# Kernel optimization log

Hardware: AMD Instinct MI355X
Metric: run time of the kernel (lower is better)

The kernel has to match this reference:

```python
import jax, jax.numpy as jnp
import numpy as np

ALPHA = 0.1   # alpha_factor
BETA = 1.0    # beta_factor
NUM_CLASSES = 1000
B, D = 4096, 512


def setup_inputs() -> dict:
    key = jax.random.key(0)
    ks = jax.random.split(key, 7)
    return {
        "anchor": jax.random.normal(ks[0], (B, D), dtype=jnp.float32),
        "positive": jax.random.normal(ks[1], (B, D), dtype=jnp.float32),
        "negative": jax.random.normal(ks[2], (B, D), dtype=jnp.float32),
        "outputs": jax.random.normal(ks[3], (3 * B, NUM_CLASSES), dtype=jnp.float32),
        "labels_anchor": jax.random.randint(ks[4], (B,), 0, NUM_CLASSES, dtype=jnp.int32).astype(jnp.int64),
        "labels_neg": jax.random.randint(ks[5], (B,), 0, NUM_CLASSES, dtype=jnp.int32).astype(jnp.int64),
        "exemplars": jax.random.normal(ks[6], (NUM_CLASSES, D), dtype=jnp.float32),
    }


def reference(anchor, positive, negative, outputs, labels_anchor, labels_neg, exemplars):
    # cross-entropy (mean reduction) over concatenated labels [3B]
    labels = jnp.concatenate([labels_anchor, labels_anchor, labels_neg], axis=0)
    logp = jax.nn.log_softmax(outputs, axis=-1)                       # [3B, C]
    loss_softmax = -jnp.mean(jnp.take_along_axis(logp, labels[:, None], axis=1))

    # pairwise L2 distances anchor-to-exemplars via ||a||^2 + ||e||^2 - 2 a.e  -> [B, C]
    a_sq = jnp.sum(anchor * anchor, axis=1, keepdims=True)            # [B, 1]
    e_sq = jnp.sum(exemplars * exemplars, axis=1)[None, :]            # [1, C]
    d2 = a_sq + e_sq - 2.0 * (anchor @ exemplars.T)                   # [B, C]
    d_all = jnp.sqrt(jnp.maximum(d2, 0.0))

    d_ref = jnp.take_along_axis(d_all, labels_anchor[:, None], axis=1)[:, 0]  # [B]
    d_closest = jnp.min(d_all, axis=1)                                # [B]
    loss_center = jnp.sum(jax.nn.relu(d_ref - d_closest))

    tp = jnp.linalg.norm(anchor - positive, axis=1)                   # [B]
    tn = jnp.linalg.norm(anchor - negative, axis=1)                   # [B]
    loss_triplet = jnp.sum(jax.nn.relu(tp - tn))

    loss_total = loss_softmax + ALPHA * loss_center + BETA * loss_triplet
    return (loss_total, loss_triplet, loss_softmax, loss_center)
```

## Files before the change

### kernel.cpp

```cpp
#include <hip/hip_runtime.h>
#include <math.h>

#define BB 4096
#define DD 512
#define CC 1000

typedef __attribute__((ext_vector_type(8))) short short8;
typedef __attribute__((ext_vector_type(4))) float f32x4;

#define OFF_ABF   0
#define OFF_EBF   1048576
#define OFF_ESQ   1310720
#define OFF_ASQ   1311744
#define OFF_DREF  1315840
#define OFF_PMINP 1319936
#define OFF_CEP   1352704
#define OFF_TRP   1354240

__device__ __forceinline__ unsigned short f2bf(float x) {
    unsigned u = __float_as_uint(x);
    unsigned r = (u + 0x7FFFu + ((u >> 16) & 1u)) >> 16;
    return (unsigned short)r;
}

__global__ __launch_bounds__(512) void prep_kernel(
    const float* __restrict__ a, const float* __restrict__ ex,
    unsigned short* __restrict__ Abf, unsigned short* __restrict__ Ebf,
    float* __restrict__ esq, float* __restrict__ asq)
{
    const int bid = blockIdx.x;
    const int tid = threadIdx.x;
    const int w = tid >> 6, lane = tid & 63;

    if (bid < 512) {
        const int i = bid * 8 + w;
        const float4* ar = (const float4*)(a + (size_t)i * DD);
        float sa = 0.f;
#pragma unroll
        for (int k = 0; k < 2; k++) {
            const int j = lane + k * 64;
            float4 av = ar[j];
            union { unsigned short u[4]; uint2 q; } o;
            o.u[0]=f2bf(av.x); o.u[1]=f2bf(av.y); o.u[2]=f2bf(av.z); o.u[3]=f2bf(av.w);
            *(uint2*)(Abf + (size_t)i * DD + j * 4) = o.q;
            sa += av.x*av.x + av.y*av.y + av.z*av.z + av.w*av.w;
        }
        for (int off = 32; off; off >>= 1) sa += __shfl_xor(sa, off);
        if (lane == 0) asq[i] = sa;
    } else {
        const int c = (bid - 512) * 8 + w;
        float s = 0.f;
        if (c < CC) {
            const float4* row = (const float4*)(ex + (size_t)c * DD);
#pragma unroll
            for (int k = 0; k < 2; k++) {
                const int j = lane + k * 64;
                float4 v = row[j];
                union { unsigned short u[4]; uint2 q; } o;
                o.u[0]=f2bf(v.x); o.u[1]=f2bf(v.y); o.u[2]=f2bf(v.z); o.u[3]=f2bf(v.w);
                *(uint2*)(Ebf + (size_t)c * DD + j * 4) = o.q;
                s += v.x*v.x + v.y*v.y + v.z*v.z + v.w*v.w;
            }
            for (int off = 32; off; off >>= 1) s += __shfl_xor(s, off);
        } else {
            const uint2 z = make_uint2(0, 0);
#pragma unroll
            for (int k = 0; k < 2; k++) {
                const int j = lane + k * 64;
                *(uint2*)(Ebf + (size_t)c * DD + j * 4) = z;
            }
        }
        if (lane == 0) esq[c] = s;
    }
}

#define GL2LDS(gsrc, ldst) __builtin_amdgcn_global_load_lds( \
    (const __attribute__((address_space(1))) unsigned int*)(gsrc), \
    (__attribute__((address_space(3))) unsigned int*)(ldst), 16, 0, 0)

__global__ __launch_bounds__(512) void main_kernel(
    const unsigned short* __restrict__ Ab, const unsigned short* __restrict__ Eb,
    const float* __restrict__ asq, const float* __restrict__ esq,
    const float* __restrict__ a, const float* __restrict__ p,
    const float* __restrict__ n, const float* __restrict__ ex,
    const float* __restrict__ outp,
    const int* __restrict__ la, const int* __restrict__ ln,
    float* __restrict__ pminp, float* __restrict__ ce_part,
    float* __restrict__ tr_part, float* __restrict__ dref)
{
    __shared__ unsigned short lA[3][128 * 32];
    __shared__ unsigned short lB[3][128 * 32];
    __shared__ float s_pm[4][128];
    __shared__ float ps[8];

    const int bid = blockIdx.x;
    const int tid = threadIdx.x;
    const int w = tid >> 6, lane = tid & 63;

    if (bid < 256) {
        const int strip = bid & 31, panel = bid >> 5;
        const int gm0 = strip * 128, gn0 = panel * 128;
        const int wm = w >> 2, wn = w & 3;
        const int hi = lane >> 4, lo = lane & 15;

        const int r0 = tid >> 2, s0 = tid & 3;
        const int g0 = s0 ^ (r0 & 3);
        const size_t srcA = ((size_t)(gm0 + r0) << 9) + (g0 << 3);
        const size_t srcB = ((size_t)(gn0 + r0) << 9) + (g0 << 3);
        const int dst = tid << 3;

#define STAGE(buf, kt) do { \
        GL2LDS(Ab + srcA + ((kt) << 5), &lA[buf][dst]); \
        GL2LDS(Eb + srcB + ((kt) << 5), &lB[buf][dst]); \
    } while (0)

        f32x4 acc[4][2];
#pragma unroll
        for (int mi = 0; mi < 4; mi++)
#pragma unroll
            for (int ni = 0; ni < 2; ni++) acc[mi][ni] = (f32x4){0.f, 0.f, 0.f, 0.f};

        STAGE(0, 0);
        STAGE(1, 1);
        for (int kt = 0; kt < 16; kt++) {
            const int buf = kt % 3;
            if (kt < 14) {
                STAGE((kt + 2) % 3, kt + 2);
                asm volatile("s_waitcnt vmcnt(4)" ::: "memory");
            } else if (kt == 14) {
                asm volatile("s_waitcnt vmcnt(2)" ::: "memory");
            } else {
                asm volatile("s_waitcnt vmcnt(0)" ::: "memory");
            }
            __builtin_amdgcn_s_barrier();
            asm volatile("" ::: "memory");

            short8 af[4], bf[2];
#pragma unroll
            for (int mi = 0; mi < 4; mi++) {
                int r = (wm << 6) + (mi << 4) + lo;
                af[mi] = *(const short8*)&lA[buf][(r << 5) + ((hi ^ (r & 3)) << 3)];
            }
#pragma unroll
            for (int ni = 0; ni < 2; ni++) {
                int r = (wn << 5) + (ni << 4) + lo;
                bf[ni] = *(const short8*)&lB[buf][(r << 5) + ((hi ^ (r & 3)) << 3)];
            }
#pragma unroll
            for (int mi = 0; mi < 4; mi++)
#pragma unroll
                for (int ni = 0; ni < 2; ni++)
                    acc[mi][ni] = __builtin_amdgcn_mfma_f32_16x16x32_bf16(af[mi], bf[ni], acc[mi][ni], 0, 0, 0);

            asm volatile("" ::: "memory");
            __builtin_amdgcn_s_barrier();
        }
#undef STAGE

        float aq[4][4];
#pragma unroll
        for (int mi = 0; mi < 4; mi++) {
            float4 a0 = *(const float4*)&asq[gm0 + wm * 64 + mi * 16 + hi * 4];
            aq[mi][0]=a0.x; aq[mi][1]=a0.y; aq[mi][2]=a0.z; aq[mi][3]=a0.w;
        }
        float esqc[2]; int bad[2];
#pragma unroll
        for (int ni = 0; ni < 2; ni++) {
            int gn = gn0 + wn * 32 + ni * 16 + lo;
            esqc[ni] = esq[gn];
            bad[ni] = (gn >= CC);
        }
        float vmin[4][4];
#pragma unroll
        for (int mi = 0; mi < 4; mi++)
#pragma unroll
            for (int j = 0; j < 4; j++) {
                float best = INFINITY;
#pragma unroll
                for (int ni = 0; ni < 2; ni++) {
                    float d2 = aq[mi][j] + esqc[ni] - 2.f * acc[mi][ni][j];
                    float d = sqrtf(fmaxf(d2, 0.f));
                    if (bad[ni]) d = INFINITY;
                    best = fminf(best, d);
                }
                vmin[mi][j] = best;
            }
#pragma unroll
        for (int off = 1; off < 16; off <<= 1)
#pragma unroll
            for (int mi = 0; mi < 4; mi++)
#pragma unroll
                for (int j = 0; j < 4; j++)
                    vmin[mi][j] = fminf(vmin[mi][j], __shfl_xor(vmin[mi][j], off));

        if (lo == 0) {
#pragma unroll
            for (int mi = 0; mi < 4; mi++)
#pragma unroll
                for (int j = 0; j < 4; j++)
                    s_pm[wn][wm * 64 + mi * 16 + hi * 4 + j] = vmin[mi][j];
        }
        __syncthreads();
        if (tid < 128) {
            float m2 = fminf(fminf(s_pm[0][tid], s_pm[1][tid]),
                             fminf(s_pm[2][tid], s_pm[3][tid]));
            pminp[((size_t)(gm0 + tid) << 3) + panel] = m2;
        }
    } else if (bid < 1792) {
        const int cb = bid - 256;
        const int r = cb * 8 + w;
        const int label = (r < 2 * BB) ? la[r & (BB - 1)] : ln[r - 2 * BB];
        const float4* row4 = (const float4*)(outp + (size_t)r * CC);
        float4 v[4];
#pragma unroll
        for (int k = 0; k < 4; k++) {
            int j4 = lane + k * 64;
            v[k] = (j4 < 250) ? row4[j4]
                              : make_float4(-INFINITY, -INFINITY, -INFINITY, -INFINITY);
        }
        float m = -INFINITY;
#pragma unroll
        for (int k = 0; k < 4; k++)
            m = fmaxf(m, fmaxf(fmaxf(v[k].x, v[k].y), fmaxf(v[k].z, v[k].w)));
        for (int off = 32; off; off >>= 1) m = fmaxf(m, __shfl_xor(m, off));

        const int lj4 = label >> 2, lc = label & 3;
        float s = 0.f, lv = 0.f;
#pragma unroll
        for (int k = 0; k < 4; k++) {
            int j4 = lane + k * 64;
            s += __expf(v[k].x - m) + __expf(v[k].y - m)
               + __expf(v[k].z - m) + __expf(v[k].w - m);
            float comp = (lc == 0) ? v[k].x : (lc == 1) ? v[k].y : (lc == 2) ? v[k].z : v[k].w;
            lv += (j4 == lj4) ? comp : 0.f;
        }
        for (int off = 32; off; off >>= 1) {
            s += __shfl_xor(s, off);
            lv += __shfl_xor(lv, off);
        }
        if (lane == 0) ps[w] = -(lv - m - __logf(s));
        __syncthreads();
        if (tid == 0) {
            float t = 0.f;
#pragma unroll
            for (int q = 0; q < 8; q++) t += ps[q];
            ce_part[cb] = t;
        }
    } else {
        const int i = (bid - 1792) * 8 + w;
        const int label = la[i];
        const float4* ar = (const float4*)(a + (size_t)i * DD);
        const float4* pr = (const float4*)(p + (size_t)i * DD);
        const float4* nr = (const float4*)(n + (size_t)i * DD);
        const float4* er = (const float4*)(ex + (size_t)label * DD);
        float sp = 0.f, sn = 0.f, se = 0.f;
#pragma unroll
        for (int k = 0; k < 2; k++) {
            const int j = lane + k * 64;
            float4 av = ar[j], pv = pr[j], nv = nr[j], ev = er[j];
            float dx = av.x-pv.x, dy = av.y-pv.y, dz = av.z-pv.z, dw = av.w-pv.w;
            sp += dx*dx + dy*dy + dz*dz + dw*dw;
            dx = av.x-nv.x; dy = av.y-nv.y; dz = av.z-nv.z; dw = av.w-nv.w;
            sn += dx*dx + dy*dy + dz*dz + dw*dw;
            dx = av.x-ev.x; dy = av.y-ev.y; dz = av.z-ev.z; dw = av.w-ev.w;
            se += dx*dx + dy*dy + dz*dz + dw*dw;
        }
        for (int off = 32; off; off >>= 1) {
            sp += __shfl_xor(sp, off);
            sn += __shfl_xor(sn, off);
            se += __shfl_xor(se, off);
        }
        if (lane == 0) {
            dref[i] = sqrtf(se);
            ps[w] = fmaxf(sqrtf(sp) - sqrtf(sn), 0.f);
        }
        __syncthreads();
        if (tid == 0) {
            float t = 0.f;
#pragma unroll
            for (int q = 0; q < 8; q++) t += ps[q];
            tr_part[bid - 1792] = t;
        }
    }
}

__global__ __launch_bounds__(1024) void final_kernel(
    const float* __restrict__ ce_part, const float* __restrict__ tr_part,
    const float* __restrict__ pminp, const float* __restrict__ dref,
    float* __restrict__ out)
{
    int tid = threadIdx.x;
    float ce = ce_part[tid] + ((tid < 512) ? ce_part[tid + 1024] : 0.f);
    float tr = (tid < 512) ? tr_part[tid] : 0.f;
    float ctr = 0.f;
    float4 d4 = *(const float4*)&dref[tid * 4];
#pragma unroll
    for (int k = 0; k < 4; k++) {
        int m = tid * 4 + k;
        float4 p0 = *(const float4*)&pminp[(size_t)m * 8];
        float4 p1 = *(const float4*)&pminp[(size_t)m * 8 + 4];
        float mn = fminf(fminf(fminf(p0.x, p0.y), fminf(p0.z, p0.w)),
                         fminf(fminf(p1.x, p1.y), fminf(p1.z, p1.w)));
        float dr = (k == 0) ? d4.x : (k == 1) ? d4.y : (k == 2) ? d4.z : d4.w;
        ctr += fmaxf(dr - mn, 0.f);
    }
    for (int off = 32; off; off >>= 1) {
        ce += __shfl_xor(ce, off);
        tr += __shfl_xor(tr, off);
        ctr += __shfl_xor(ctr, off);
    }
    __shared__ float s[3][16];
    int wid = tid >> 6, lane = tid & 63;
    if (lane == 0) { s[0][wid] = ce; s[1][wid] = tr; s[2][wid] = ctr; }
    __syncthreads();
    if (tid == 0) {
        float tce = 0.f, ttr = 0.f, tctr = 0.f;
#pragma unroll
        for (int q = 0; q < 16; q++) { tce += s[0][q]; ttr += s[1][q]; tctr += s[2][q]; }
        float lsm = tce / (3.f * BB);
        out[0] = lsm + 0.1f * tctr + 1.0f * ttr;
        out[1] = ttr;
        out[2] = lsm;
        out[3] = tctr;
    }
}

extern "C" void kernel_launch(void* const* d_in, const int* in_sizes, int n_in,
                              void* d_out, int out_size, void* d_ws, size_t ws_size,
                              hipStream_t stream) {
    const float* anchor   = (const float*)d_in[0];
    const float* positive = (const float*)d_in[1];
    const float* negative = (const float*)d_in[2];
    const float* outputs  = (const float*)d_in[3];
    const int*   la       = (const int*)d_in[4];
    const int*   ln       = (const int*)d_in[5];
    const float* ex       = (const float*)d_in[6];
    float* out = (float*)d_out;
    float* ws  = (float*)d_ws;

    unsigned short* Abf = (unsigned short*)(ws + OFF_ABF);
    unsigned short* Ebf = (unsigned short*)(ws + OFF_EBF);
    float* esq      = ws + OFF_ESQ;
    float* asq      = ws + OFF_ASQ;
    float* dref     = ws + OFF_DREF;
    float* pminp    = ws + OFF_PMINP;
    float* ce_part  = ws + OFF_CEP;
    float* tr_part  = ws + OFF_TRP;

    hipLaunchKernelGGL(prep_kernel,  dim3(640),  dim3(512),  0, stream,
                       anchor, ex, Abf, Ebf, esq, asq);
    hipLaunchKernelGGL(main_kernel,  dim3(2304), dim3(512),  0, stream,
                       Abf, Ebf, asq, esq, anchor, positive, negative, ex,
                       outputs, la, ln, pminp, ce_part, tr_part, dref);
    hipLaunchKernelGGL(final_kernel, dim3(1),    dim3(1024), 0, stream,
                       ce_part, tr_part, pminp, dref, out);
}
```

Measured before the change: 32.98 us.

## Fuse triplet/dref work into prep kernel and load GEMM fragments directly from global

The triplet and reference-distance computation moves into the prep kernel's anchor blocks, which already read the anchor rows, so the anchor is read once instead of twice and main_kernel has fewer blocks. The GEMM path drops its LDS triple-buffered global_load_lds pipeline and barriers. Each wave now loads its bf16 MFMA fragments straight from global memory, relying on L2/L1 for reuse. This removes the LDS usage and synchronisation, at the cost of redundant global loads across waves and less latency hiding.

Measured after the change: 46.08 us. 39.7% more time.

```diff
diff --git a/kernel.cpp b/kernel.cpp
--- a/kernel.cpp
+++ b/kernel.cpp
@@ -24,29 +24,59 @@
 }
 
 __global__ __launch_bounds__(512) void prep_kernel(
-    const float* __restrict__ a, const float* __restrict__ ex,
+    const float* __restrict__ a, const float* __restrict__ p,
+    const float* __restrict__ n, const float* __restrict__ ex,
+    const int* __restrict__ la,
     unsigned short* __restrict__ Abf, unsigned short* __restrict__ Ebf,
-    float* __restrict__ esq, float* __restrict__ asq)
+    float* __restrict__ esq, float* __restrict__ asq,
+    float* __restrict__ dref, float* __restrict__ tr_part)
 {
+    __shared__ float ps[8];
     const int bid = blockIdx.x;
     const int tid = threadIdx.x;
     const int w = tid >> 6, lane = tid & 63;
 
     if (bid < 512) {
         const int i = bid * 8 + w;
+        const int label = la[i];
         const float4* ar = (const float4*)(a + (size_t)i * DD);
-        float sa = 0.f;
+        const float4* pr = (const float4*)(p + (size_t)i * DD);
+        const float4* nr = (const float4*)(n + (size_t)i * DD);
+        const float4* er = (const float4*)(ex + (size_t)label * DD);
+        float sa = 0.f, sp = 0.f, sn = 0.f, se = 0.f;
 #pragma unroll
         for (int k = 0; k < 2; k++) {
             const int j = lane + k * 64;
-            float4 av = ar[j];
+            float4 av = ar[j], pv = pr[j], nv = nr[j], ev = er[j];
             union { unsigned short u[4]; uint2 q; } o;
             o.u[0]=f2bf(av.x); o.u[1]=f2bf(av.y); o.u[2]=f2bf(av.z); o.u[3]=f2bf(av.w);
             *(uint2*)(Abf + (size_t)i * DD + j * 4) = o.q;
             sa += av.x*av.x + av.y*av.y + av.z*av.z + av.w*av.w;
-        }
-        for (int off = 32; off; off >>= 1) sa += __shfl_xor(sa, off);
-        if (lane == 0) asq[i] = sa;
+            float dx = av.x-pv.x, dy = av.y-pv.y, dz = av.z-pv.z, dw = av.w-pv.w;
+            sp += dx*dx + dy*dy + dz*dz + dw*dw;
+            dx = av.x-nv.x; dy = av.y-nv.y; dz = av.z-nv.z; dw = av.w-nv.w;
+            sn += dx*dx + dy*dy + dz*dz + dw*dw;
+            dx = av.x-ev.x; dy = av.y-ev.y; dz = av.z-ev.z; dw = av.w-ev.w;
+            se += dx*dx + dy*dy + dz*dz + dw*dw;
+        }
+        for (int off = 32; off; off >>= 1) {
+            sa += __shfl_xor(sa, off);
+            sp += __shfl_xor(sp, off);
+            sn += __shfl_xor(sn, off);
+            se += __shfl_xor(se, off);
+        }
+        if (lane == 0) {
+            asq[i]  = sa;
+            dref[i] = sqrtf(se);
+            ps[w] = fmaxf(sqrtf(sp) - sqrtf(sn), 0.f);
+        }
+        __syncthreads();
+        if (tid == 0) {
+            float t = 0.f;
+#pragma unroll
+            for (int q = 0; q < 8; q++) t += ps[q];
+            tr_part[bid] = t;
+        }
     } else {
         const int c = (bid - 512) * 8 + w;
         float s = 0.f;
@@ -74,22 +104,13 @@
     }
 }
 
-#define GL2LDS(gsrc, ldst) __builtin_amdgcn_global_load_lds( \
-    (const __attribute__((address_space(1))) unsigned int*)(gsrc), \
-    (__attribute__((address_space(3))) unsigned int*)(ldst), 16, 0, 0)
-
 __global__ __launch_bounds__(512) void main_kernel(
     const unsigned short* __restrict__ Ab, const unsigned short* __restrict__ Eb,
     const float* __restrict__ asq, const float* __restrict__ esq,
-    const float* __restrict__ a, const float* __restrict__ p,
-    const float* __restrict__ n, const float* __restrict__ ex,
     const float* __restrict__ outp,
     const int* __restrict__ la, const int* __restrict__ ln,
-    float* __restrict__ pminp, float* __restrict__ ce_part,
-    float* __restrict__ tr_part, float* __restrict__ dref)
+    float* __restrict__ pminp, float* __restrict__ ce_part)
 {
-    __shared__ unsigned short lA[3][128 * 32];
-    __shared__ unsigned short lB[3][128 * 32];
     __shared__ float s_pm[4][128];
     __shared__ float ps[8];
 
@@ -103,16 +124,14 @@
         const int wm = w >> 2, wn = w & 3;
         const int hi = lane >> 4, lo = lane & 15;
 
-        const int r0 = tid >> 2, s0 = tid & 3;
-        const int g0 = s0 ^ (r0 & 3);
-        const size_t srcA = ((size_t)(gm0 + r0) << 9) + (g0 << 3);
-        const size_t srcB = ((size_t)(gn0 + r0) << 9) + (g0 << 3);
-        const int dst = tid << 3;
-
-#define STAGE(buf, kt) do { \
-        GL2LDS(Ab + srcA + ((kt) << 5), &lA[buf][dst]); \
-        GL2LDS(Eb + srcB + ((kt) << 5), &lB[buf][dst]); \
-    } while (0)
+        const unsigned short* pa[4];
+#pragma unroll
+        for (int mi = 0; mi < 4; mi++)
+            pa[mi] = Ab + ((size_t)(gm0 + wm * 64 + mi * 16 + lo) << 9) + (hi << 3);
+        const unsigned short* pb[2];
+#pragma unroll
+        for (int ni = 0; ni < 2; ni++)
+            pb[ni] = Eb + ((size_t)(gn0 + wn * 32 + ni * 16 + lo) << 9) + (hi << 3);
 
         f32x4 acc[4][2];
 #pragma unroll
@@ -120,42 +139,21 @@
 #pragma unroll
             for (int ni = 0; ni < 2; ni++) acc[mi][ni] = (f32x4){0.f, 0.f, 0.f, 0.f};
 
-        STAGE(0, 0);
-        STAGE(1, 1);
-        for (int kt = 0; kt < 16; kt++) {
-            const int buf = kt % 3;
-            if (kt < 14) {
-                STAGE((kt + 2) % 3, kt + 2);
-                asm volatile("s_waitcnt vmcnt(4)" ::: "memory");
-            } else if (kt == 14) {
-                asm volatile("s_waitcnt vmcnt(2)" ::: "memory");
-            } else {
-                asm volatile("s_waitcnt vmcnt(0)" ::: "memory");
-            }
-            __builtin_amdgcn_s_barrier();
-            asm volatile("" ::: "memory");
-
+#pragma unroll 4
+        for (int kk = 0; kk < 16; kk++) {
             short8 af[4], bf[2];
 #pragma unroll
-            for (int mi = 0; mi < 4; mi++) {
-                int r = (wm << 6) + (mi << 4) + lo;
-                af[mi] = *(const short8*)&lA[buf][(r << 5) + ((hi ^ (r & 3)) << 3)];
-            }
-#pragma unroll
-            for (int ni = 0; ni < 2; ni++) {
-                int r = (wn << 5) + (ni << 4) + lo;
-                bf[ni] = *(const short8*)&lB[buf][(r << 5) + ((hi ^ (r & 3)) << 3)];
-            }
+            for (int mi = 0; mi < 4; mi++)
+                af[mi] = *(const short8*)(pa[mi] + (kk << 5));
+#pragma unroll
+            for (int ni = 0; ni < 2; ni++)
+                bf[ni] = *(const short8*)(pb[ni] + (kk << 5));
 #pragma unroll
             for (int mi = 0; mi < 4; mi++)
 #pragma unroll
                 for (int ni = 0; ni < 2; ni++)
                     acc[mi][ni] = __builtin_amdgcn_mfma_f32_16x16x32_bf16(af[mi], bf[ni], acc[mi][ni], 0, 0, 0);
-
-            asm volatile("" ::: "memory");
-            __builtin_amdgcn_s_barrier();
-        }
-#undef STAGE
+        }
 
         float aq[4][4];
 #pragma unroll
@@ -206,7 +204,7 @@
                              fminf(s_pm[2][tid], s_pm[3][tid]));
             pminp[((size_t)(gm0 + tid) << 3) + panel] = m2;
         }
-    } else if (bid < 1792) {
+    } else {
         const int cb = bid - 256;
         const int r = cb * 8 + w;
         const int label = (r < 2 * BB) ? la[r & (BB - 1)] : ln[r - 2 * BB];
@@ -245,41 +243,6 @@
 #pragma unroll
             for (int q = 0; q < 8; q++) t += ps[q];
             ce_part[cb] = t;
-        }
-    } else {
-        const int i = (bid - 1792) * 8 + w;
-        const int label = la[i];
-        const float4* ar = (const float4*)(a + (size_t)i * DD);
-        const float4* pr = (const float4*)(p + (size_t)i * DD);
-        const float4* nr = (const float4*)(n + (size_t)i * DD);
-        const float4* er = (const float4*)(ex + (size_t)label * DD);
-        float sp = 0.f, sn = 0.f, se = 0.f;
-#pragma unroll
-        for (int k = 0; k < 2; k++) {
-            const int j = lane + k * 64;
-            float4 av = ar[j], pv = pr[j], nv = nr[j], ev = er[j];
-            float dx = av.x-pv.x, dy = av.y-pv.y, dz = av.z-pv.z, dw = av.w-pv.w;
-            sp += dx*dx + dy*dy + dz*dz + dw*dw;
-            dx = av.x-nv.x; dy = av.y-nv.y; dz = av.z-nv.z; dw = av.w-nv.w;
-            sn += dx*dx + dy*dy + dz*dz + dw*dw;
-            dx = av.x-ev.x; dy = av.y-ev.y; dz = av.z-ev.z; dw = av.w-ev.w;
-            se += dx*dx + dy*dy + dz*dz + dw*dw;
-        }
-        for (int off = 32; off; off >>= 1) {
-            sp += __shfl_xor(sp, off);
-            sn += __shfl_xor(sn, off);
-            se += __shfl_xor(se, off);
-        }
-        if (lane == 0) {
-            dref[i] = sqrtf(se);
-            ps[w] = fmaxf(sqrtf(sp) - sqrtf(sn), 0.f);
-        }
-        __syncthreads();
-        if (tid == 0) {
-            float t = 0.f;
-#pragma unroll
-            for (int q = 0; q < 8; q++) t += ps[q];
-            tr_part[bid - 1792] = t;
         }
     }
 }
@@ -348,10 +311,9 @@
     float* tr_part  = ws + OFF_TRP;
 
     hipLaunchKernelGGL(prep_kernel,  dim3(640),  dim3(512),  0, stream,
-                       anchor, ex, Abf, Ebf, esq, asq);
-    hipLaunchKernelGGL(main_kernel,  dim3(2304), dim3(512),  0, stream,
-                       Abf, Ebf, asq, esq, anchor, positive, negative, ex,
-                       outputs, la, ln, pminp, ce_part, tr_part, dref);
+                       anchor, positive, negative, ex, la, Abf, Ebf, esq, asq, dref, tr_part);
+    hipLaunchKernelGGL(main_kernel,  dim3(1792), dim3(512),  0, stream,
+                       Abf, Ebf, asq, esq, outputs, la, ln, pminp, ce_part);
     hipLaunchKernelGGL(final_kernel, dim3(1),    dim3(1024), 0, stream,
                        ce_part, tr_part, pminp, dref, out);
 }
```

## Replace triple-buffered K=32 pipeline with single-buffered K=64 tiles

Applied to the files above, without the earlier changes.

The GEMM main loop no longer uses a 3-stage ring of K=32 LDS buffers with prefetch two tiles ahead. Each step now loads one K=64 tile per operand into a single buffer with an 8-way XOR swizzle, waits for it fully, then runs two MFMA sub-steps. This halves the loop trip count and barrier count and cuts LDS usage, which may allow more resident blocks. The cost is that global-to-LDS loads are no longer overlapped with compute inside a block, so latency is exposed on every iteration.

Result: slower. 36.57 us (+10.9%).

```diff
diff --git a/kernel.cpp b/kernel.cpp
--- a/kernel.cpp
+++ b/kernel.cpp
@@ -88,8 +88,8 @@
     float* __restrict__ pminp, float* __restrict__ ce_part,
     float* __restrict__ tr_part, float* __restrict__ dref)
 {
-    __shared__ unsigned short lA[3][128 * 32];
-    __shared__ unsigned short lB[3][128 * 32];
+    __shared__ unsigned short lA[128 * 64];
+    __shared__ unsigned short lB[128 * 64];
     __shared__ float s_pm[4][128];
     __shared__ float ps[8];
 
@@ -103,16 +103,14 @@
         const int wm = w >> 2, wn = w & 3;
         const int hi = lane >> 4, lo = lane & 15;
 
-        const int r0 = tid >> 2, s0 = tid & 3;
-        const int g0 = s0 ^ (r0 & 3);
-        const size_t srcA = ((size_t)(gm0 + r0) << 9) + (g0 << 3);
-        const size_t srcB = ((size_t)(gn0 + r0) << 9) + (g0 << 3);
-        const int dst = tid << 3;
-
-#define STAGE(buf, kt) do { \
-        GL2LDS(Ab + srcA + ((kt) << 5), &lA[buf][dst]); \
-        GL2LDS(Eb + srcB + ((kt) << 5), &lB[buf][dst]); \
-    } while (0)
+        size_t srcA[2], srcB[2]; int dst2[2];
+#pragma unroll
+        for (int i = 0; i < 2; i++) {
+            int c = tid + i * 512, r = c >> 3, s = c & 7;
+            srcA[i] = ((size_t)(gm0 + r) << 9) + ((s ^ (r & 7)) << 3);
+            srcB[i] = ((size_t)(gn0 + r) << 9) + ((s ^ (r & 7)) << 3);
+            dst2[i] = c << 3;
+        }
 
         f32x4 acc[4][2];
 #pragma unroll
@@ -120,42 +118,38 @@
 #pragma unroll
             for (int ni = 0; ni < 2; ni++) acc[mi][ni] = (f32x4){0.f, 0.f, 0.f, 0.f};
 
-        STAGE(0, 0);
-        STAGE(1, 1);
-        for (int kt = 0; kt < 16; kt++) {
-            const int buf = kt % 3;
-            if (kt < 14) {
-                STAGE((kt + 2) % 3, kt + 2);
-                asm volatile("s_waitcnt vmcnt(4)" ::: "memory");
-            } else if (kt == 14) {
-                asm volatile("s_waitcnt vmcnt(2)" ::: "memory");
-            } else {
-                asm volatile("s_waitcnt vmcnt(0)" ::: "memory");
-            }
+        for (int kt = 0; kt < 8; kt++) {
+#pragma unroll
+            for (int i = 0; i < 2; i++) {
+                GL2LDS(Ab + srcA[i] + (kt << 6), &lA[dst2[i]]);
+                GL2LDS(Eb + srcB[i] + (kt << 6), &lB[dst2[i]]);
+            }
+            asm volatile("s_waitcnt vmcnt(0)" ::: "memory");
             __builtin_amdgcn_s_barrier();
             asm volatile("" ::: "memory");
 
-            short8 af[4], bf[2];
-#pragma unroll
-            for (int mi = 0; mi < 4; mi++) {
-                int r = (wm << 6) + (mi << 4) + lo;
-                af[mi] = *(const short8*)&lA[buf][(r << 5) + ((hi ^ (r & 3)) << 3)];
-            }
-#pragma unroll
-            for (int ni = 0; ni < 2; ni++) {
-                int r = (wn << 5) + (ni << 4) + lo;
-                bf[ni] = *(const short8*)&lB[buf][(r << 5) + ((hi ^ (r & 3)) << 3)];
-            }
-#pragma unroll
-            for (int mi = 0; mi < 4; mi++)
-#pragma unroll
-                for (int ni = 0; ni < 2; ni++)
-                    acc[mi][ni] = __builtin_amdgcn_mfma_f32_16x16x32_bf16(af[mi], bf[ni], acc[mi][ni], 0, 0, 0);
-
+#pragma unroll
+            for (int kk = 0; kk < 2; kk++) {
+                short8 af[4], bf[2];
+#pragma unroll
+                for (int mi = 0; mi < 4; mi++) {
+                    int r = (wm << 6) + (mi << 4) + lo, s = (kk << 2) + hi;
+                    af[mi] = *(const short8*)&lA[(r << 6) + ((s ^ (r & 7)) << 3)];
+                }
+#pragma unroll
+                for (int ni = 0; ni < 2; ni++) {
+                    int r = (wn << 5) + (ni << 4) + lo, s = (kk << 2) + hi;
+                    bf[ni] = *(const short8*)&lB[(r << 6) + ((s ^ (r & 7)) << 3)];
+                }
+#pragma unroll
+                for (int mi = 0; mi < 4; mi++)
+#pragma unroll
+                    for (int ni = 0; ni < 2; ni++)
+                        acc[mi][ni] = __builtin_amdgcn_mfma_f32_16x16x32_bf16(af[mi], bf[ni], acc[mi][ni], 0, 0, 0);
+            }
             asm volatile("" ::: "memory");
             __builtin_amdgcn_s_barrier();
         }
-#undef STAGE
 
         float aq[4][4];
 #pragma unroll
```
